# Performance work log

Hardware: AMD Instinct MI355X
Metric: run time of the kernel (lower is better)

Reference implementation:

```python
import jax, jax.numpy as jnp
from jax import lax
import numpy as np

T, B, S, D, H, NC = 10, 16, 200, 768, 300, 4


def setup_inputs() -> dict:
    key = jax.random.key(0)
    ks = jax.random.split(key, 20)
    f = lambda k, shp: jax.random.normal(k, shp, dtype=jnp.float32)
    u = lambda k, shp: jax.random.uniform(k, shp, dtype=jnp.float32)
    return {
        "input_ids": jax.random.randint(ks[0], (B, T, 16), 0, 50265),
        "sequence_list": f(ks[1], (T, B, S, D)),
        "start_probs": u(ks[2], (T, B, S)),
        "end_probs": u(ks[3], (T, B, S)),
        "classification_probs": u(ks[4], (T, B, NC)),
        "before_state_start_probs": u(ks[5], (T, B, S)),
        "before_state_end_probs": u(ks[6], (T, B, S)),
        "before_state_classification_probs": u(ks[7], (T, B, NC)),
        "unk_mask": u(ks[8], (B, T, S)),
        "none_mask": u(ks[9], (B, T, S)),
        "ans_mask": u(ks[10], (B, T, S)),
        "Wih_f": f(ks[11], (4 * H, 5 * D)) * 0.02,
        "Whh_f": f(ks[12], (4 * H, H)) * 0.02,
        "bih_f": jnp.zeros((4 * H,), jnp.float32),
        "bhh_f": jnp.zeros((4 * H,), jnp.float32),
        "Wih_b": f(ks[13], (4 * H, 5 * D)) * 0.02,
        "Whh_b": f(ks[14], (4 * H, H)) * 0.02,
        "bih_b": jnp.zeros((4 * H,), jnp.float32),
        "bhh_b": jnp.zeros((4 * H,), jnp.float32),
        "Wcls": f(ks[15], (NC, S * 2 * H)) * 0.005,
        "bcls": jnp.zeros((NC,), jnp.float32),
    }


def _attn_weight(p, c, am, um, nm):
    # p: [B,S] probs; c: [B,NC] class probs; masks [B,S]
    # sum of three masked weighted copies collapses to one fused weight
    return p * (am * c[:, 0:1] + um * c[:, 1:2] + nm * c[:, 2:3])


def _lstm_dir(zx, Whh, bhh, h0, c0):
    # zx: [S,B,4H] precomputed x @ Wih.T + bih (big GEMM outside the scan)
    def step(carry, zt):
        h, c = carry
        z = zt + h @ Whh.T + bhh
        i, f, g, o = jnp.split(z, 4, axis=-1)  # torch gate order i,f,g,o
        c = jax.nn.sigmoid(f) * c + jax.nn.sigmoid(i) * jnp.tanh(g)
        h = jax.nn.sigmoid(o) * jnp.tanh(c)
        return (h, c), h
    (h, c), ys = lax.scan(step, (h0, c0), zx)
    return ys, h, c


def reference(input_ids, sequence_list, start_probs, end_probs, classification_probs,
              before_state_start_probs, before_state_end_probs, before_state_classification_probs,
              unk_mask, none_mask, ans_mask,
              Wih_f, Whh_f, bih_f, bhh_f, Wih_b, Whh_b, bih_b, bhh_b, Wcls, bcls):
    T_, B_, S_ = start_probs.shape
    H_ = Whh_f.shape[-1]
    amT = jnp.swapaxes(ans_mask, 0, 1)   # [T,B,S]
    umT = jnp.swapaxes(unk_mask, 0, 1)
    nmT = jnp.swapaxes(none_mask, 0, 1)
    # before-state attention (only step 0's probs are used, per the original code)
    bss = _attn_weight(before_state_start_probs[0], before_state_classification_probs[0],
                       amT[0], umT[0], nmT[0])[..., None] * sequence_list[0]
    bse = _attn_weight(before_state_end_probs[0], before_state_classification_probs[0],
                       amT[0], umT[0], nmT[0])[..., None] * sequence_list[0]
    z0 = jnp.zeros((B_, H_), start_probs.dtype)

    def outer(carry, xs):
        prev_s, prev_e, hf, cf, hb, cb = carry
        sp, ep, cp, am, um, nm, seq = xs
        s_att = _attn_weight(sp, cp, am, um, nm)[..., None] * seq  # [B,S,D]
        e_att = _attn_weight(ep, cp, am, um, nm)[..., None] * seq
        rnn_in = jnp.concatenate([seq, s_att, e_att, prev_s, prev_e], axis=-1)  # [B,S,5D]
        xT = jnp.swapaxes(rnn_in, 0, 1)  # [S,B,5D]
        zf = xT @ Wih_f.T + bih_f        # [S,B,4H]
        zb = xT[::-1] @ Wih_b.T + bih_b
        yf, hf, cf = _lstm_dir(zf, Whh_f, bhh_f, hf, cf)
        yb, hb, cb = _lstm_dir(zb, Whh_b, bhh_b, hb, cb)
        y = jnp.concatenate([yf, yb[::-1]], axis=-1)            # [S,B,2H]
        y = jnp.swapaxes(y, 0, 1).reshape(B_, -1)               # [B,S*2H]
        logits = jax.nn.relu(y) @ Wcls.T + bcls                 # [B,NC]
        return (s_att, e_att, hf, cf, hb, cb), logits

    init = (bss, bse, z0, z0, z0, z0)
    xs = (start_probs, end_probs, classification_probs, amT, umT, nmT, sequence_list)
    _, logits = lax.scan(outer, init, xs)
    return logits  # [T,B,NC]
```

## Files before the change

kernel.cpp:

```cpp
#include <hip/hip_runtime.h>
#include <stdint.h>
#include <stdio.h>

#define T_ 10
#define B_ 16
#define S_ 200
#define D_ 768
#define H_ 300
#define NC_ 4
#define M_ (S_ * B_)
#define K5_ (5 * D_)
#define N2_ 2400
#define G4_ 1200
#define HXW_SLOT 2432
#define HLDS_STRIDE 344
#define NTILE 130

typedef unsigned short u16;
typedef unsigned int u32;
typedef __attribute__((ext_vector_type(8))) short short8;
typedef __attribute__((ext_vector_type(4))) float float4v;
typedef __attribute__((ext_vector_type(4))) unsigned int u32x4;

static __device__ __forceinline__ u16 f2bf(float x) {
  union { float f; u32 u; } v; v.f = x;
  u32 u = v.u;
  u32 r = (u + 0x7FFFu + ((u >> 16) & 1u)) >> 16;
  return (u16)r;
}

static __device__ __forceinline__ void async16(const void* g, void* l) {
  __builtin_amdgcn_global_load_lds((const __attribute__((address_space(1))) u32*)g,
                                   (__attribute__((address_space(3))) u32*)l, 16, 0, 0);
}

static __device__ __forceinline__ float sigmoid_f(float x) {
  return 1.f / (1.f + __expf(-x));
}
static __device__ __forceinline__ float tanh_f(float x) {
  float e = __expf(2.f * x);
  return 1.f - 2.f / (e + 1.f);
}

__global__ void k_prep_s(const float* __restrict__ seq,
                         const float* __restrict__ sp, const float* __restrict__ ep,
                         const float* __restrict__ cp,
                         const float* __restrict__ bsp, const float* __restrict__ bep,
                         const float* __restrict__ bcp,
                         const float* __restrict__ um, const float* __restrict__ nm,
                         const float* __restrict__ am,
                         u16* __restrict__ s0, u16* __restrict__ sa, u16* __restrict__ sb,
                         u16* __restrict__ sa0, u16* __restrict__ sb0) {
  int bid = blockIdx.x;
  int tid = threadIdx.x;
  if (bid < T_ * M_) {
    int t = bid / M_;
    int r = bid % M_;
    int s = r >> 4, b = r & 15;
    float c0 = cp[(t * B_ + b) * NC_ + 0];
    float c1 = cp[(t * B_ + b) * NC_ + 1];
    float c2 = cp[(t * B_ + b) * NC_ + 2];
    int mi = (b * T_ + t) * S_ + s;
    float w = am[mi] * c0 + um[mi] * c1 + nm[mi] * c2;
    float aw = sp[(t * B_ + b) * S_ + s] * w;
    float bw = ep[(t * B_ + b) * S_ + s] * w;
    const float* x = seq + ((size_t)(t * B_ + b) * S_ + s) * D_;
    size_t ob = (size_t)bid * D_;
    for (int d = tid; d < D_; d += 256) {
      float xv = x[d];
      s0[ob + d] = f2bf(xv);
      sa[ob + d] = f2bf(aw * xv);
      sb[ob + d] = f2bf(bw * xv);
    }
  } else {
    int r = bid - T_ * M_;
    int s = r >> 4, b = r & 15;
    float c0 = bcp[b * NC_ + 0], c1 = bcp[b * NC_ + 1], c2 = bcp[b * NC_ + 2];
    int mi = (b * T_ + 0) * S_ + s;
    float w = am[mi] * c0 + um[mi] * c1 + nm[mi] * c2;
    float aw = bsp[b * S_ + s] * w;
    float bw = bep[b * S_ + s] * w;
    const float* x = seq + ((size_t)b * S_ + s) * D_;
    size_t ob = (size_t)r * D_;
    for (int d = tid; d < D_; d += 256) {
      float xv = x[d];
      sa0[ob + d] = f2bf(aw * xv);
      sb0[ob + d] = f2bf(bw * xv);
    }
  }
}

__global__ void k_prep_w(const float* __restrict__ wf, const float* __restrict__ wb,
                         const float* __restrict__ whf, const float* __restrict__ whb,
                         const float* __restrict__ bihf, const float* __restrict__ bhhf,
                         const float* __restrict__ bihb, const float* __restrict__ bhhb,
                         const float* __restrict__ bcls,
                         u16* __restrict__ wcat, u16* __restrict__ whh,
                         float* __restrict__ bias, float* __restrict__ outp,
                         u32* __restrict__ hxw, u32* __restrict__ tagb) {
  int bid = blockIdx.x, tid = threadIdx.x;
  if (bid < N2_) {
    const float* src = bid < G4_ ? wf + (size_t)bid * K5_ : wb + (size_t)(bid - G4_) * K5_;
    u16* dst = wcat + (size_t)bid * K5_;
    for (int k = tid; k < K5_; k += 256) dst[k] = f2bf(src[k]);
  } else if (bid < N2_ + 2 * G4_) {
    int r = bid - N2_;
    int dir = r / G4_, n = r % G4_;
    const float* src = (dir ? whb : whf) + (size_t)n * H_;
    u16* dst = whh + (size_t)(dir * G4_ + n) * 320;
    for (int k = tid; k < 320; k += 256) dst[k] = (k < H_) ? f2bf(src[k]) : (u16)0;
  } else {
    for (int i = tid; i < 2 * G4_; i += 256) {
      int dir = i / G4_, n = i % G4_;
      bias[i] = dir ? (bihb[n] + bhhb[n]) : (bihf[n] + bhhf[n]);
    }
    for (int i = tid; i < T_ * B_ * NC_; i += 256) outp[i] = bcls[i & 3];
    for (int i = tid; i < 2 * 2 * HXW_SLOT; i += 256) hxw[i] = 0;
    if (tid < 32) tagb[tid] = 0;
  }
}

__global__ __launch_bounds__(1024) void k_main(
    const u16* __restrict__ s0, const u16* __restrict__ sa, const u16* __restrict__ sb,
    const u16* __restrict__ sa0, const u16* __restrict__ sb0,
    const u16* __restrict__ wcat, float* __restrict__ zbase,
    const u16* __restrict__ whh, const float* __restrict__ bias,
    const float* __restrict__ wcls, u32* __restrict__ hxw, u32* __restrict__ tagb,
    float* __restrict__ outp, float* __restrict__ cst,
    int t_lstm, int t_gemm, int steady) {
  __shared__ __align__(16) char lds_raw[32768];

  int tid = threadIdx.x;
  int lane = tid & 63, wv = tid >> 6;
  int bid = (int)blockIdx.x;

  int dir = 0, w = 0, tile = -1;
  bool lstm_role = false;
  if (steady) {
    int grp = bid >> 3, sub = bid & 7;
    if (sub < 2) {
      if (grp < 5) { lstm_role = true; dir = sub; w = grp; }
      else return;
    } else {
      if (t_gemm < 0) return;
      tile = grp * 6 + (sub - 2);
      if (tile >= NTILE) return;
    }
  } else {
    tile = bid;
  }

  if (!lstm_role) {
    int mt = tile % 13, nt = tile / 13;
    int m0 = mt * 256, n0 = nt * 256;
    u16* As = (u16*)lds_raw;
    u16* Bs = (u16*)(lds_raw + 16384);
    int wm = wv & 3, wn = wv >> 2;

    const u16* ap[5];
    ap[0] = s0 + (size_t)t_gemm * M_ * D_;
    ap[1] = sa + (size_t)t_gemm * M_ * D_;
    ap[2] = sb + (size_t)t_gemm * M_ * D_;
    ap[3] = t_gemm ? sa + (size_t)(t_gemm - 1) * M_ * D_ : sa0;
    ap[4] = t_gemm ? sb + (size_t)(t_gemm - 1) * M_ * D_ : sb0;
    float* z = zbase + (size_t)(t_gemm & 1) * M_ * N2_;

    float4v acc[4][4];
#pragma unroll
    for (int i = 0; i < 4; i++)
#pragma unroll
      for (int j = 0; j < 4; j++) acc[i][j] = (float4v){0.f, 0.f, 0.f, 0.f};

    int rowA = tid >> 2;
    int seg = tid & 3;
    int mr = m0 + rowA; if (mr > M_ - 1) mr = M_ - 1;
    int nr = n0 + rowA; if (nr > N2_ - 1) nr = N2_ - 1;

    for (int which = 0; which < 5; ++which) {
      const u16* ab = which == 0 ? ap[0] : which == 1 ? ap[1] : which == 2 ? ap[2]
                      : which == 3 ? ap[3] : ap[4];
      for (int kk = 0; kk < 24; ++kk) {
        int kof = kk * 32;
        async16(ab + (size_t)mr * D_ + kof + seg * 8, As + wv * 512);
        async16(wcat + (size_t)nr * K5_ + which * D_ + kof + seg * 8, Bs + wv * 512);
        __syncthreads();
        short8 af[4], bf[4];
#pragma unroll
        for (int i = 0; i < 4; i++) {
          af[i] = *(const short8*)&As[(wm * 64 + i * 16 + (lane & 15)) * 32 + (lane >> 4) * 8];
          bf[i] = *(const short8*)&Bs[(wn * 64 + i * 16 + (lane & 15)) * 32 + (lane >> 4) * 8];
        }
#pragma unroll
        for (int i = 0; i < 4; i++)
#pragma unroll
          for (int j = 0; j < 4; j++)
            acc[i][j] = __builtin_amdgcn_mfma_f32_16x16x32_bf16(af[i], bf[j], acc[i][j], 0, 0, 0);
        __syncthreads();
      }
    }
#pragma unroll
    for (int i = 0; i < 4; i++) {
      int m = m0 + wm * 64 + i * 16 + (lane >> 4) * 4;
#pragma unroll
      for (int j = 0; j < 4; j++) {
        int n = n0 + wn * 64 + j * 16 + (lane & 15);
        if (n < N2_) {
#pragma unroll
          for (int r = 0; r < 4; r++)
            if (m + r < M_) z[(size_t)(m + r) * N2_ + n] = acc[i][j][r];
        }
      }
    }
    return;
  }

  u16* h_lds = (u16*)lds_raw;
  u32* h32 = (u32*)lds_raw;
  float* smem = (float*)(lds_raw + 16 * HLDS_STRIDE * 2);

  int t = t_lstm;
  int wgid = dir * 5 + w;
  int gate = wv >> 2, q = wv & 3;
  const float* z = zbase + (size_t)(t & 1) * M_ * N2_;

  short8 bfr[10];
  {
    int col = lane & 15;
    int u = w * 64 + q * 16 + col;
    int krow = (lane >> 4) * 8;
    if (u < H_) {
      const u16* base = whh + (size_t)(dir * G4_ + gate * H_ + u) * 320 + krow;
#pragma unroll
      for (int kk = 0; kk < 10; ++kk) bfr[kk] = *(const short8*)(base + kk * 32);
    } else {
#pragma unroll
      for (int kk = 0; kk < 10; ++kk) bfr[kk] = (short8){0, 0, 0, 0, 0, 0, 0, 0};
    }
  }

  int b = tid >> 6;
  int u_loc = tid & 63;
  int u_glob = w * 64 + u_loc;
  bool active = u_glob < H_;
  float bias_r[4];
#pragma unroll
  for (int g = 0; g < 4; ++g)
    bias_r[g] = active ? bias[dir * G4_ + g * H_ + u_glob] : 0.f;

  float c_state = t > 0 ? cst[wgid * 1024 + tid] : 0.f;
  float clsacc[4] = {0.f, 0.f, 0.f, 0.f};

  for (int i = tid; i < 16 * HLDS_STRIDE; i += 1024) h_lds[i] = 0;
  __syncthreads();

  u32* hx_base = hxw + dir * 2 * HXW_SLOT;
  u32* tag_base = tagb + dir * 16;

  bool rd_on = tid < 608;
  int rdw = tid * 4;
  int rlofs[4];
  u32 rmask = 0;
#pragma unroll
  for (int k = 0; k < 4; ++k) {
    int i = rdw + k;
    rlofs[k] = 0;
    if (rd_on && i < 2432) {
      int bb = i / 152;
      int jj = i - bb * 152;
      if (jj < 150) { rlofs[k] = bb * 172 + jj; rmask |= 1u << k; }
    }
  }

  for (int s_mod = 0; s_mod < S_; ++s_mod) {
    int g = t * S_ + s_mod;
    int s_in = dir ? (S_ - 1 - s_mod) : s_mod;

    float z_in[4] = {0.f, 0.f, 0.f, 0.f}, wc[4] = {0.f, 0.f, 0.f, 0.f};
    if (active) {
      const float* zr = z + (size_t)(s_in * B_ + b) * N2_ + dir * G4_;
      int ycol = s_in * 600 + dir * H_ + u_glob;
#pragma unroll
      for (int gg = 0; gg < 4; ++gg) z_in[gg] = zr[gg * H_ + u_glob];
#pragma unroll
      for (int n = 0; n < 4; ++n) wc[n] = wcls[(size_t)n * (S_ * 600) + ycol];
    }

    if (g > 0) {
      const u32* tp0 = tag_base;
      const u32* tp4 = tag_base + 4;
      int tries = 0;
      for (;;) {
        u32x4 tA; u32 tB;
        asm volatile("global_load_dwordx4 %0, %2, off sc1\n\t"
                     "global_load_dword %1, %3, off sc1\n\t"
                     "s_waitcnt vmcnt(0)"
                     : "=&v"(tA), "=&v"(tB) : "v"(tp0), "v"(tp4) : "memory");
        if (tA[0] >= (u32)g && tA[1] >= (u32)g && tA[2] >= (u32)g &&
            tA[3] >= (u32)g && tB >= (u32)g) break;
        if (++tries >= (1 << 20)) break;
      }
      __builtin_amdgcn_sched_barrier(0);
      const u32* src = hx_base + (g & 1) * HXW_SLOT;
      if (rd_on) {
        u32x4 d;
        asm volatile("global_load_dwordx4 %0, %1, off sc1\n\t"
                     "s_waitcnt vmcnt(0)"
                     : "=&v"(d) : "v"(src + rdw) : "memory");
#pragma unroll
        for (int k = 0; k < 4; ++k)
          if (rmask & (1u << k)) h32[rlofs[k]] = d[k];
      }
      __syncthreads();
    }

    {
      float4v acc = (float4v){0.f, 0.f, 0.f, 0.f};
      int m = lane & 15;
      int kbase = (lane >> 4) * 8;
      const u16* hl = h_lds + m * HLDS_STRIDE + kbase;
#pragma unroll
      for (int kk = 0; kk < 10; ++kk) {
        short8 af = *(const short8*)(hl + kk * 32);
        acc = __builtin_amdgcn_mfma_f32_16x16x32_bf16(af, bfr[kk], acc, 0, 0, 0);
      }
      int col = lane & 15;
      int rb = (lane >> 4) * 4;
#pragma unroll
      for (int r = 0; r < 4; r++)
        smem[(gate * 16 + rb + r) * 65 + q * 16 + col] = acc[r];
    }
    __syncthreads();

    {
      float zi = smem[(0 * 16 + b) * 65 + u_loc] + z_in[0] + bias_r[0];
      float zf = smem[(1 * 16 + b) * 65 + u_loc] + z_in[1] + bias_r[1];
      float zg = smem[(2 * 16 + b) * 65 + u_loc] + z_in[2] + bias_r[2];
      float zo = smem[(3 * 16 + b) * 65 + u_loc] + z_in[3] + bias_r[3];
      float ig = sigmoid_f(zi);
      float fg = sigmoid_f(zf);
      float gg = tanh_f(zg);
      float og = sigmoid_f(zo);
      c_state = fg * c_state + ig * gg;
      float hval = og * tanh_f(c_state);
      u16 hb = f2bf(hval);
      u32 mine = (u32)hb;
      u32 other = (u32)__shfl_xor((int)mine, 1);
      if (active) {
        h_lds[b * HLDS_STRIDE + u_glob] = hb;
        float rv = hval > 0.f ? hval : 0.f;
#pragma unroll
        for (int n = 0; n < 4; ++n) clsacc[n] += rv * wc[n];
      }
      if (active && !(u_loc & 1)) {
        u32 wrd = mine | (other << 16);
        __hip_atomic_store(&hx_base[((g + 1) & 1) * HXW_SLOT + b * 152 + (u_glob >> 1)],
                           wrd, __ATOMIC_RELAXED, __HIP_MEMORY_SCOPE_AGENT);
      }
    }
    __syncthreads();
    if (tid == 0)
      __hip_atomic_store(&tag_base[w], (u32)(g + 1),
                         __ATOMIC_RELAXED, __HIP_MEMORY_SCOPE_AGENT);

    if (s_mod == S_ - 1) {
      __syncthreads();
#pragma unroll
      for (int n = 0; n < 4; ++n) smem[(b * 64 + u_loc) * 4 + n] = clsacc[n];
      __syncthreads();
      if (tid < B_ * NC_) {
        int bb = tid >> 2, n = tid & 3;
        float s = 0.f;
        for (int u = 0; u < 64; ++u) s += smem[(bb * 64 + u) * 4 + n];
        atomicAdd(&outp[(t * B_ + bb) * NC_ + n], s);
      }
    }
  }
  cst[wgid * 1024 + tid] = c_state;
}

extern "C" void kernel_launch(void* const* d_in, const int* in_sizes, int n_in,
                              void* d_out, int out_size, void* d_ws, size_t ws_size,
                              hipStream_t stream) {
  const float* seq = (const float*)d_in[1];
  const float* sp = (const float*)d_in[2];
  const float* ep = (const float*)d_in[3];
  const float* cp = (const float*)d_in[4];
  const float* bsp = (const float*)d_in[5];
  const float* bep = (const float*)d_in[6];
  const float* bcp = (const float*)d_in[7];
  const float* um = (const float*)d_in[8];
  const float* nm = (const float*)d_in[9];
  const float* am = (const float*)d_in[10];
  const float* wihf = (const float*)d_in[11];
  const float* whhf = (const float*)d_in[12];
  const float* bihf = (const float*)d_in[13];
  const float* bhhf = (const float*)d_in[14];
  const float* wihb = (const float*)d_in[15];
  const float* whhb = (const float*)d_in[16];
  const float* bihb = (const float*)d_in[17];
  const float* bhhb = (const float*)d_in[18];
  const float* wcls = (const float*)d_in[19];
  const float* bcls = (const float*)d_in[20];

  char* ws = (char*)d_ws;
  size_t off = 0;
  auto alloc = [&](size_t bytes) -> char* {
    char* p = ws + off;
    off += (bytes + 255) & ~(size_t)255;
    return p;
  };
  u16* S0 = (u16*)alloc((size_t)T_ * M_ * D_ * 2);
  u16* SA = (u16*)alloc((size_t)T_ * M_ * D_ * 2);
  u16* SB = (u16*)alloc((size_t)T_ * M_ * D_ * 2);
  u16* SA0 = (u16*)alloc((size_t)M_ * D_ * 2);
  u16* SB0 = (u16*)alloc((size_t)M_ * D_ * 2);
  u16* WCAT = (u16*)alloc((size_t)N2_ * K5_ * 2);
  u16* WHH = (u16*)alloc((size_t)2 * G4_ * 320 * 2);
  float* BIAS = (float*)alloc((size_t)2 * G4_ * 4);
  float* Z = (float*)alloc((size_t)2 * M_ * N2_ * 4);
  u32* HXW = (u32*)alloc((size_t)2 * 2 * HXW_SLOT * 4);
  u32* TAGB = (u32*)alloc((size_t)32 * 4);
  float* CST = (float*)alloc((size_t)10 * 1024 * 4);

  if (off > ws_size) {
    fprintf(stderr, "[kernel] ws too small: need %zu, have %zu\n", off, ws_size);
    return;
  }

  hipLaunchKernelGGL(k_prep_s, dim3(T_ * M_ + M_), dim3(256), 0, stream,
                     seq, sp, ep, cp, bsp, bep, bcp, um, nm, am, S0, SA, SB, SA0, SB0);
  hipLaunchKernelGGL(k_prep_w, dim3(N2_ + 2 * G4_ + 1), dim3(256), 0, stream,
                     wihf, wihb, whhf, whhb, bihf, bhhf, bihb, bhhb, bcls,
                     WCAT, WHH, BIAS, (float*)d_out, HXW, TAGB);
  hipLaunchKernelGGL(k_main, dim3(NTILE), dim3(1024), 0, stream,
                     S0, SA, SB, SA0, SB0, WCAT, Z, WHH, BIAS, wcls, HXW, TAGB,
                     (float*)d_out, CST, 0, 0, 0);
  for (int t = 0; t < T_; ++t) {
    hipLaunchKernelGGL(k_main, dim3(176), dim3(1024), 0, stream,
                       S0, SA, SB, SA0, SB0, WCAT, Z, WHH, BIAS, wcls, HXW, TAGB,
                       (float*)d_out, CST, t, (t < T_ - 1) ? t + 1 : -1, 1);
  }
}
```

Measured before the change: 6.096 ms.

## Run both LSTM directions in one workgroup per unit slice, interleaving steps

Each LSTM workgroup now handles both the forward and backward directions for its unit slice, alternating their steps within one loop. The backward wait on the cross-workgroup tag is overlapped with the forward step's compute. This halves the number of LSTM workgroups, which frees compute units for the concurrent GEMM tiles, and hides one direction's spin latency behind the other's work. The cost is a longer serial chain per workgroup, twice the weight registers, and a more intricate tag protocol that could deadlock or race if the ordering is wrong.

```diff
diff --git a/kernel.cpp b/kernel.cpp
--- a/kernel.cpp
+++ b/kernel.cpp
@@ -128,23 +128,25 @@
     const float* __restrict__ wcls, u32* __restrict__ hxw, u32* __restrict__ tagb,
     float* __restrict__ outp, float* __restrict__ cst,
     int t_lstm, int t_gemm, int steady) {
-  __shared__ __align__(16) char lds_raw[32768];
+  __shared__ __align__(16) char lds_raw[40960];
 
   int tid = threadIdx.x;
   int lane = tid & 63, wv = tid >> 6;
   int bid = (int)blockIdx.x;
 
-  int dir = 0, w = 0, tile = -1;
+  int w = 0, tile = -1;
   bool lstm_role = false;
   if (steady) {
     int grp = bid >> 3, sub = bid & 7;
-    if (sub < 2) {
-      if (grp < 5) { lstm_role = true; dir = sub; w = grp; }
+    if (sub == 0) {
+      if (grp < 5) { lstm_role = true; w = grp; }
       else return;
-    } else {
+    } else if (sub >= 2) {
       if (t_gemm < 0) return;
       tile = grp * 6 + (sub - 2);
       if (tile >= NTILE) return;
+    } else {
+      return;
     }
   } else {
     tile = bid;
@@ -214,27 +216,30 @@
     return;
   }
 
-  u16* h_lds = (u16*)lds_raw;
-  u32* h32 = (u32*)lds_raw;
-  float* smem = (float*)(lds_raw + 16 * HLDS_STRIDE * 2);
+  u16* h_lds0 = (u16*)lds_raw;
+  u16* h_lds1 = (u16*)(lds_raw + 11008);
+  u32* h32_0 = (u32*)lds_raw;
+  u32* h32_1 = (u32*)(lds_raw + 11008);
+  float* smem = (float*)(lds_raw + 22016);
 
   int t = t_lstm;
-  int wgid = dir * 5 + w;
+  int base = t * S_;
   int gate = wv >> 2, q = wv & 3;
   const float* z = zbase + (size_t)(t & 1) * M_ * N2_;
 
-  short8 bfr[10];
-  {
+  short8 bfr[2][10];
+#pragma unroll
+  for (int d = 0; d < 2; ++d) {
     int col = lane & 15;
     int u = w * 64 + q * 16 + col;
     int krow = (lane >> 4) * 8;
     if (u < H_) {
-      const u16* base = whh + (size_t)(dir * G4_ + gate * H_ + u) * 320 + krow;
-#pragma unroll
-      for (int kk = 0; kk < 10; ++kk) bfr[kk] = *(const short8*)(base + kk * 32);
+      const u16* bw_ = whh + (size_t)(d * G4_ + gate * H_ + u) * 320 + krow;
+#pragma unroll
+      for (int kk = 0; kk < 10; ++kk) bfr[d][kk] = *(const short8*)(bw_ + kk * 32);
     } else {
 #pragma unroll
-      for (int kk = 0; kk < 10; ++kk) bfr[kk] = (short8){0, 0, 0, 0, 0, 0, 0, 0};
+      for (int kk = 0; kk < 10; ++kk) bfr[d][kk] = (short8){0, 0, 0, 0, 0, 0, 0, 0};
     }
   }
 
@@ -242,19 +247,25 @@
   int u_loc = tid & 63;
   int u_glob = w * 64 + u_loc;
   bool active = u_glob < H_;
-  float bias_r[4];
-#pragma unroll
-  for (int g = 0; g < 4; ++g)
-    bias_r[g] = active ? bias[dir * G4_ + g * H_ + u_glob] : 0.f;
-
-  float c_state = t > 0 ? cst[wgid * 1024 + tid] : 0.f;
-  float clsacc[4] = {0.f, 0.f, 0.f, 0.f};
-
-  for (int i = tid; i < 16 * HLDS_STRIDE; i += 1024) h_lds[i] = 0;
+  float bias_r[2][4];
+#pragma unroll
+  for (int d = 0; d < 2; ++d)
+#pragma unroll
+    for (int g = 0; g < 4; ++g)
+      bias_r[d][g] = active ? bias[d * G4_ + g * H_ + u_glob] : 0.f;
+
+  float cs0 = t > 0 ? cst[(0 * 5 + w) * 1024 + tid] : 0.f;
+  float cs1 = t > 0 ? cst[(1 * 5 + w) * 1024 + tid] : 0.f;
+  float cls0[4] = {0.f, 0.f, 0.f, 0.f};
+  float cls1[4] = {0.f, 0.f, 0.f, 0.f};
+
+  for (int i = tid; i < 5504; i += 1024) { h_lds0[i] = 0; h_lds1[i] = 0; }
   __syncthreads();
 
-  u32* hx_base = hxw + dir * 2 * HXW_SLOT;
-  u32* tag_base = tagb + dir * 16;
+  u32* hx0 = hxw;
+  u32* hx1 = hxw + 2 * HXW_SLOT;
+  u32* tg0 = tagb;
+  u32* tg1 = tagb + 16;
 
   bool rd_on = tid < 608;
   int rdw = tid * 4;
@@ -272,56 +283,56 @@
   }
 
   for (int s_mod = 0; s_mod < S_; ++s_mod) {
-    int g = t * S_ + s_mod;
-    int s_in = dir ? (S_ - 1 - s_mod) : s_mod;
-
-    float z_in[4] = {0.f, 0.f, 0.f, 0.f}, wc[4] = {0.f, 0.f, 0.f, 0.f};
+    int g = base + s_mod;
+    int s_in0 = s_mod;
+    int s_in1 = S_ - 1 - s_mod;
+
+    float z0v[4] = {0.f, 0.f, 0.f, 0.f}, wc0[4] = {0.f, 0.f, 0.f, 0.f};
     if (active) {
-      const float* zr = z + (size_t)(s_in * B_ + b) * N2_ + dir * G4_;
-      int ycol = s_in * 600 + dir * H_ + u_glob;
-#pragma unroll
-      for (int gg = 0; gg < 4; ++gg) z_in[gg] = zr[gg * H_ + u_glob];
-#pragma unroll
-      for (int n = 0; n < 4; ++n) wc[n] = wcls[(size_t)n * (S_ * 600) + ycol];
-    }
-
+      const float* zr = z + (size_t)(s_in0 * B_ + b) * N2_;
+      int ycol = s_in0 * 600 + u_glob;
+#pragma unroll
+      for (int gg = 0; gg < 4; ++gg) z0v[gg] = zr[gg * H_ + u_glob];
+#pragma unroll
+      for (int n = 0; n < 4; ++n) wc0[n] = wcls[(size_t)n * (S_ * 600) + ycol];
+    }
     if (g > 0) {
-      const u32* tp0 = tag_base;
-      const u32* tp4 = tag_base + 4;
       int tries = 0;
       for (;;) {
         u32x4 tA; u32 tB;
         asm volatile("global_load_dwordx4 %0, %2, off sc1\n\t"
                      "global_load_dword %1, %3, off sc1\n\t"
                      "s_waitcnt vmcnt(0)"
-                     : "=&v"(tA), "=&v"(tB) : "v"(tp0), "v"(tp4) : "memory");
+                     : "=&v"(tA), "=&v"(tB) : "v"(tg0), "v"(tg0 + 4) : "memory");
         if (tA[0] >= (u32)g && tA[1] >= (u32)g && tA[2] >= (u32)g &&
             tA[3] >= (u32)g && tB >= (u32)g) break;
         if (++tries >= (1 << 20)) break;
       }
       __builtin_amdgcn_sched_barrier(0);
-      const u32* src = hx_base + (g & 1) * HXW_SLOT;
+      const u32* src = hx0 + (g & 1) * HXW_SLOT;
       if (rd_on) {
-        u32x4 d;
+        u32x4 dd;
         asm volatile("global_load_dwordx4 %0, %1, off sc1\n\t"
                      "s_waitcnt vmcnt(0)"
-                     : "=&v"(d) : "v"(src + rdw) : "memory");
+                     : "=&v"(dd) : "v"(src + rdw) : "memory");
 #pragma unroll
         for (int k = 0; k < 4; ++k)
-          if (rmask & (1u << k)) h32[rlofs[k]] = d[k];
-      }
-      __syncthreads();
-    }
+          if (rmask & (1u << k)) h32_0[rlofs[k]] = dd[k];
+      }
+    }
+    __syncthreads();
+    if (tid == 0)
+      __hip_atomic_store(&tg1[w], (u32)g, __ATOMIC_RELAXED, __HIP_MEMORY_SCOPE_AGENT);
 
     {
       float4v acc = (float4v){0.f, 0.f, 0.f, 0.f};
       int m = lane & 15;
       int kbase = (lane >> 4) * 8;
-      const u16* hl = h_lds + m * HLDS_STRIDE + kbase;
+      const u16* hl = h_lds0 + m * HLDS_STRIDE + kbase;
 #pragma unroll
       for (int kk = 0; kk < 10; ++kk) {
         short8 af = *(const short8*)(hl + kk * 32);
-        acc = __builtin_amdgcn_mfma_f32_16x16x32_bf16(af, bfr[kk], acc, 0, 0, 0);
+        acc = __builtin_amdgcn_mfma_f32_16x16x32_bf16(af, bfr[0][kk], acc, 0, 0, 0);
       }
       int col = lane & 15;
       int rb = (lane >> 4) * 4;
@@ -332,40 +343,114 @@
     __syncthreads();
 
     {
-      float zi = smem[(0 * 16 + b) * 65 + u_loc] + z_in[0] + bias_r[0];
-      float zf = smem[(1 * 16 + b) * 65 + u_loc] + z_in[1] + bias_r[1];
-      float zg = smem[(2 * 16 + b) * 65 + u_loc] + z_in[2] + bias_r[2];
-      float zo = smem[(3 * 16 + b) * 65 + u_loc] + z_in[3] + bias_r[3];
-      float ig = sigmoid_f(zi);
-      float fg = sigmoid_f(zf);
-      float gg = tanh_f(zg);
-      float og = sigmoid_f(zo);
-      c_state = fg * c_state + ig * gg;
-      float hval = og * tanh_f(c_state);
+      float zi = smem[(0 * 16 + b) * 65 + u_loc] + z0v[0] + bias_r[0][0];
+      float zf = smem[(1 * 16 + b) * 65 + u_loc] + z0v[1] + bias_r[0][1];
+      float zg = smem[(2 * 16 + b) * 65 + u_loc] + z0v[2] + bias_r[0][2];
+      float zo = smem[(3 * 16 + b) * 65 + u_loc] + z0v[3] + bias_r[0][3];
+      float ig = sigmoid_f(zi), fg = sigmoid_f(zf);
+      float gg = tanh_f(zg), og = sigmoid_f(zo);
+      cs0 = fg * cs0 + ig * gg;
+      float hval = og * tanh_f(cs0);
       u16 hb = f2bf(hval);
       u32 mine = (u32)hb;
       u32 other = (u32)__shfl_xor((int)mine, 1);
       if (active) {
-        h_lds[b * HLDS_STRIDE + u_glob] = hb;
+        h_lds0[b * HLDS_STRIDE + u_glob] = hb;
         float rv = hval > 0.f ? hval : 0.f;
 #pragma unroll
-        for (int n = 0; n < 4; ++n) clsacc[n] += rv * wc[n];
+        for (int n = 0; n < 4; ++n) cls0[n] += rv * wc0[n];
       }
       if (active && !(u_loc & 1)) {
         u32 wrd = mine | (other << 16);
-        __hip_atomic_store(&hx_base[((g + 1) & 1) * HXW_SLOT + b * 152 + (u_glob >> 1)],
+        __hip_atomic_store(&hx0[((g + 1) & 1) * HXW_SLOT + b * 152 + (u_glob >> 1)],
                            wrd, __ATOMIC_RELAXED, __HIP_MEMORY_SCOPE_AGENT);
+      }
+    }
+
+    float z1v[4] = {0.f, 0.f, 0.f, 0.f}, wc1[4] = {0.f, 0.f, 0.f, 0.f};
+    if (active) {
+      const float* zr = z + (size_t)(s_in1 * B_ + b) * N2_ + G4_;
+      int ycol = s_in1 * 600 + H_ + u_glob;
+#pragma unroll
+      for (int gg = 0; gg < 4; ++gg) z1v[gg] = zr[gg * H_ + u_glob];
+#pragma unroll
+      for (int n = 0; n < 4; ++n) wc1[n] = wcls[(size_t)n * (S_ * 600) + ycol];
+    }
+    if (g > 0) {
+      int tries = 0;
+      for (;;) {
+        u32x4 tA; u32 tB;
+        asm volatile("global_load_dwordx4 %0, %2, off sc1\n\t"
+                     "global_load_dword %1, %3, off sc1\n\t"
+                     "s_waitcnt vmcnt(0)"
+                     : "=&v"(tA), "=&v"(tB) : "v"(tg1), "v"(tg1 + 4) : "memory");
+        if (tA[0] >= (u32)g && tA[1] >= (u32)g && tA[2] >= (u32)g &&
+            tA[3] >= (u32)g && tB >= (u32)g) break;
+        if (++tries >= (1 << 20)) break;
+      }
+      __builtin_amdgcn_sched_barrier(0);
+      const u32* src = hx1 + (g & 1) * HXW_SLOT;
+      if (rd_on) {
+        u32x4 dd;
+        asm volatile("global_load_dwordx4 %0, %1, off sc1\n\t"
+                     "s_waitcnt vmcnt(0)"
+                     : "=&v"(dd) : "v"(src + rdw) : "memory");
+#pragma unroll
+        for (int k = 0; k < 4; ++k)
+          if (rmask & (1u << k)) h32_1[rlofs[k]] = dd[k];
       }
     }
     __syncthreads();
     if (tid == 0)
-      __hip_atomic_store(&tag_base[w], (u32)(g + 1),
-                         __ATOMIC_RELAXED, __HIP_MEMORY_SCOPE_AGENT);
+      __hip_atomic_store(&tg0[w], (u32)(g + 1), __ATOMIC_RELAXED, __HIP_MEMORY_SCOPE_AGENT);
+
+    {
+      float4v acc = (float4v){0.f, 0.f, 0.f, 0.f};
+      int m = lane & 15;
+      int kbase = (lane >> 4) * 8;
+      const u16* hl = h_lds1 + m * HLDS_STRIDE + kbase;
+#pragma unroll
+      for (int kk = 0; kk < 10; ++kk) {
+        short8 af = *(const short8*)(hl + kk * 32);
+        acc = __builtin_amdgcn_mfma_f32_16x16x32_bf16(af, bfr[1][kk], acc, 0, 0, 0);
+      }
+      int col = lane & 15;
+      int rb = (lane >> 4) * 4;
+#pragma unroll
+      for (int r = 0; r < 4; r++)
+        smem[(gate * 16 + rb + r) * 65 + q * 16 + col] = acc[r];
+    }
+    __syncthreads();
+
+    {
+      float zi = smem[(0 * 16 + b) * 65 + u_loc] + z1v[0] + bias_r[1][0];
+      float zf = smem[(1 * 16 + b) * 65 + u_loc] + z1v[1] + bias_r[1][1];
+      float zg = smem[(2 * 16 + b) * 65 + u_loc] + z1v[2] + bias_r[1][2];
+      float zo = smem[(3 * 16 + b) * 65 + u_loc] + z1v[3] + bias_r[1][3];
+      float ig = sigmoid_f(zi), fg = sigmoid_f(zf);
+      float gg = tanh_f(zg), og = sigmoid_f(zo);
+      cs1 = fg * cs1 + ig * gg;
+      float hval = og * tanh_f(cs1);
+      u16 hb = f2bf(hval);
+      u32 mine = (u32)hb;
+      u32 other = (u32)__shfl_xor((int)mine, 1);
+      if (active) {
+        h_lds1[b * HLDS_STRIDE + u_glob] = hb;
+        float rv = hval > 0.f ? hval : 0.f;
+#pragma unroll
+        for (int n = 0; n < 4; ++n) cls1[n] += rv * wc1[n];
+      }
+      if (active && !(u_loc & 1)) {
+        u32 wrd = mine | (other << 16);
+        __hip_atomic_store(&hx1[((g + 1) & 1) * HXW_SLOT + b * 152 + (u_glob >> 1)],
+                           wrd, __ATOMIC_RELAXED, __HIP_MEMORY_SCOPE_AGENT);
+      }
+    }
 
     if (s_mod == S_ - 1) {
       __syncthreads();
 #pragma unroll
-      for (int n = 0; n < 4; ++n) smem[(b * 64 + u_loc) * 4 + n] = clsacc[n];
+      for (int n = 0; n < 4; ++n) smem[(b * 64 + u_loc) * 4 + n] = cls0[n];
       __syncthreads();
       if (tid < B_ * NC_) {
         int bb = tid >> 2, n = tid & 3;
@@ -373,9 +458,23 @@
         for (int u = 0; u < 64; ++u) s += smem[(bb * 64 + u) * 4 + n];
         atomicAdd(&outp[(t * B_ + bb) * NC_ + n], s);
       }
-    }
-  }
-  cst[wgid * 1024 + tid] = c_state;
+      __syncthreads();
+#pragma unroll
+      for (int n = 0; n < 4; ++n) smem[(b * 64 + u_loc) * 4 + n] = cls1[n];
+      __syncthreads();
+      if (tid < B_ * NC_) {
+        int bb = tid >> 2, n = tid & 3;
+        float s = 0.f;
+        for (int u = 0; u < 64; ++u) s += smem[(bb * 64 + u) * 4 + n];
+        atomicAdd(&outp[(t * B_ + bb) * NC_ + n], s);
+      }
+    }
+  }
+  __syncthreads();
+  if (tid == 0)
+    __hip_atomic_store(&tg1[w], (u32)(base + S_), __ATOMIC_RELAXED, __HIP_MEMORY_SCOPE_AGENT);
+  cst[(0 * 5 + w) * 1024 + tid] = cs0;
+  cst[(1 * 5 + w) * 1024 + tid] = cs1;
 }
 
 extern "C" void kernel_launch(void* const* d_in, const int* in_sizes, int n_in,
```

After: 15.27 ms. 150% more time.
